# Kernel tuning notes

Hardware: AMD Instinct MI355X
Metric: run time of the kernel (lower is better)

## Reference

```python
import jax, jax.numpy as jnp
import numpy as np

N = 100000
E = 3200000
F_IN = 512
NUM_CLASSES = 8
H1, C1 = 4, 8   # conv1: 4 heads, 8 channels each (concat -> 32)
H2, C2 = 1, NUM_CLASSES  # conv2: 1 head, mean (concat=False)
NEG_SLOPE = 0.2


def gat_conv(x, W, att_src, att_dst, bias, src, dst, num_nodes, concat):
    """PyG-style GATConv (eval mode, self-loops already in src/dst)."""
    H, C = att_src.shape
    xp = (x @ W).reshape(-1, H, C)              # [N, H, C]
    a_s = (xp * att_src[None]).sum(-1)           # [N, H]
    a_d = (xp * att_dst[None]).sum(-1)           # [N, H]
    e = jax.nn.leaky_relu(a_s[src] + a_d[dst], NEG_SLOPE)  # [E, H]
    # segment softmax over destination nodes (stable)
    e_max = jax.ops.segment_max(e, dst, num_segments=num_nodes)
    e = jnp.exp(e - e_max[dst])
    denom = jax.ops.segment_sum(e, dst, num_segments=num_nodes)
    alpha = e / denom[dst]                        # [E, H]
    msg = xp[src] * alpha[..., None]              # [E, H, C]
    out = jax.ops.segment_sum(msg, dst, num_segments=num_nodes)  # [N, H, C]
    if concat:
        out = out.reshape(num_nodes, H * C)
    else:
        out = out.mean(axis=1)
    return out + bias


def setup_inputs() -> dict:
    key = jax.random.key(0)
    ks = jax.random.split(key, 9)
    s = 0.1
    return {
        "x": jax.random.normal(ks[0], (N, F_IN), dtype=jnp.float32),
        "edge_index": jax.random.randint(ks[1], (2, E), 0, N, dtype=jnp.int32),
        "W1": jax.random.normal(ks[2], (F_IN, H1 * C1), dtype=jnp.float32) * s,
        "att_src1": jax.random.normal(ks[3], (H1, C1), dtype=jnp.float32) * s,
        "att_dst1": jax.random.normal(ks[4], (H1, C1), dtype=jnp.float32) * s,
        "b1": jnp.zeros((H1 * C1,), dtype=jnp.float32),
        "W2": jax.random.normal(ks[5], (H1 * C1, H2 * C2), dtype=jnp.float32) * s,
        "att_src2": jax.random.normal(ks[6], (H2, C2), dtype=jnp.float32) * s,
        "att_dst2": jax.random.normal(ks[7], (H2, C2), dtype=jnp.float32) * s,
        "b2": jnp.zeros((C2,), dtype=jnp.float32),
    }


def reference(x, edge_index, W1, att_src1, att_dst1, b1, W2, att_src2, att_dst2, b2):
    # PyG GATConv default add_self_loops=True
    loop = jnp.arange(N, dtype=edge_index.dtype)
    src = jnp.concatenate([edge_index[0], loop])
    dst = jnp.concatenate([edge_index[1], loop])
    # dropout is identity in eval mode
    h = jax.nn.elu(gat_conv(x, W1, att_src1, att_dst1, b1, src, dst, N, True))
    out = gat_conv(h, W2, att_src2, att_dst2, b2, src, dst, N, False)
    return out
```

## Files before the change

### kernel.cpp

```cpp
#include <hip/hip_runtime.h>

typedef unsigned short u16;
typedef unsigned int   u32;

#define NN  100000
#define EE  3200000
#define ETOT 3300000
#define FIN 512
#define NBUK 1024
#define NPB  98
#define CAP  4096
#define TILE_A 2048
#define NBLK_A ((ETOT + TILE_A - 1) / TILE_A)
#define NBLK_G ((NN + 63) / 64)

typedef __attribute__((ext_vector_type(8))) short bfx8;
typedef __attribute__((ext_vector_type(4))) float f32x4;

__device__ __forceinline__ float bf2f(u16 u){ return __uint_as_float(((u32)u) << 16); }
__device__ __forceinline__ float lo16f(u32 v){ return __uint_as_float(v << 16); }
__device__ __forceinline__ float hi16f(u32 v){ return __uint_as_float(v & 0xffff0000u); }
__device__ __forceinline__ u16 f2bf(float f){
  u32 u = __float_as_uint(f);
  u += 0x7fffu + ((u >> 16) & 1u);
  return (u16)(u >> 16);
}
__device__ __forceinline__ u32 pack2(float a, float b){
  return ((u32)f2bf(b) << 16) | (u32)f2bf(a);
}

__device__ __forceinline__ void binA_body(int blk, const int* __restrict__ ei,
                                          u32* __restrict__ gcnt,
                                          u32* __restrict__ buk,
                                          u32* hcnt, u32* hbase){
  int t = threadIdx.x;
  hcnt[t] = 0; hcnt[t + 256] = 0; hcnt[t + 512] = 0; hcnt[t + 768] = 0;
  __syncthreads();
  int e0 = blk * TILE_A;
  u32 pk[8], meta[8];
  #pragma unroll
  for (int i = 0; i < 8; i++){
    int e = e0 + i*256 + t;
    if (e < ETOT){
      int s, d;
      if (e < EE){ s = ei[e]; d = ei[EE + e]; } else { s = e - EE; d = s; }
      u32 b = (u32)d / NPB;
      pk[i] = ((u32)(d - (int)b*NPB) << 17) | (u32)s;
      u32 r = atomicAdd(&hcnt[b], 1u);
      meta[i] = (b << 11) | r;
    } else meta[i] = 0xFFFFFFFFu;
  }
  __syncthreads();
  for (int q = t; q < NBUK; q += 256){
    u32 c = hcnt[q];
    if (c) hbase[q] = atomicAdd(&gcnt[q], c);
  }
  __syncthreads();
  #pragma unroll
  for (int i = 0; i < 8; i++){
    if (meta[i] != 0xFFFFFFFFu){
      u32 b = meta[i] >> 11, r = meta[i] & 2047u;
      buk[((u32)b << 12) + hbase[b] + r] = pk[i];
    }
  }
}

__device__ __forceinline__ void gemm_body(int gb,
    const float* __restrict__ x, const u16* __restrict__ WTb,
    const float* __restrict__ attS, const float* __restrict__ attD,
    u16* __restrict__ xp1, float* __restrict__ as1, float* __restrict__ ad1){
  int tid = threadIdx.x;
  int nb  = gb * 64;

  int lane = tid & 63, wid = tid >> 6;
  int m = lane & 15, quad = lane >> 4;
  int rowbase = wid * 16;
  int row = nb + rowbase + m; if (row >= NN) row = NN - 1;
  const float* xrow = x + (size_t)row * FIN + quad * 8;
  const u16* b0g = WTb + m * FIN + quad * 8;
  const u16* b1g = b0g + 16 * FIN;

  f32x4 acc0 = {0.f, 0.f, 0.f, 0.f};
  f32x4 acc1 = {0.f, 0.f, 0.f, 0.f};

  union Ubf { bfx8 v; u32 u[4]; };

  #pragma unroll
  for (int kc = 0; kc < 4; kc++){
    #pragma unroll
    for (int ks = 0; ks < 4; ks++){
      const float4* g = (const float4*)(xrow + kc*128 + ks*32);
      float4 f0 = g[0], f1 = g[1];
      Ubf ua;
      ua.u[0] = pack2(f0.x, f0.y); ua.u[1] = pack2(f0.z, f0.w);
      ua.u[2] = pack2(f1.x, f1.y); ua.u[3] = pack2(f1.z, f1.w);
      bfx8 b0 = *(const bfx8*)(b0g + kc*128 + ks*32);
      bfx8 b1 = *(const bfx8*)(b1g + kc*128 + ks*32);
      acc0 = __builtin_amdgcn_mfma_f32_16x16x32_bf16(ua.v, b0, acc0, 0, 0, 0);
      acc1 = __builtin_amdgcn_mfma_f32_16x16x32_bf16(ua.v, b1, acc1, 0, 0, 0);
    }
  }

  #pragma unroll
  for (int t = 0; t < 2; t++){
    f32x4 acc = t ? acc1 : acc0;
    int colg = t*16 + m;
    float aS = attS[colg], aD = attD[colg];
    #pragma unroll
    for (int r = 0; r < 4; r++){
      int node = nb + rowbase + quad*4 + r;
      float v = acc[r];
      if (node < NN) xp1[(size_t)node*32 + colg] = f2bf(v);
      float ps = v * aS, pd = v * aD;
      ps += __shfl_xor(ps, 1); ps += __shfl_xor(ps, 2); ps += __shfl_xor(ps, 4);
      pd += __shfl_xor(pd, 1); pd += __shfl_xor(pd, 2); pd += __shfl_xor(pd, 4);
      if ((m & 7) == 0 && node < NN){
        as1[node*4 + (colg >> 3)] = ps;
        ad1[node*4 + (colg >> 3)] = pd;
      }
    }
  }
}


__global__ void __launch_bounds__(256) k_fat(const int* __restrict__ ei,
    u32* __restrict__ gcnt, u32* __restrict__ buk,
    const float* __restrict__ x, const u16* __restrict__ WTb,
    const float* __restrict__ attS, const float* __restrict__ attD,
    u16* __restrict__ xp1, float* __restrict__ as1, float* __restrict__ ad1){
  __shared__ u32 sm[NBUK*2];
  if (blockIdx.x < NBLK_A)
    binA_body(blockIdx.x, ei, gcnt, buk, sm, sm + NBUK);
  else
    gemm_body(blockIdx.x - NBLK_A, x, WTb, attS, attD, xp1, as1, ad1);
}

__global__ void __launch_bounds__(256) k_binA(const int* __restrict__ ei,
                                              u32* __restrict__ gcnt,
                                              u32* __restrict__ buk){
  __shared__ u32 sm2[NBUK*2];
  binA_body(blockIdx.x, ei, gcnt, buk, sm2, sm2 + NBUK);
}

__global__ void __launch_bounds__(256) k_gemm1(
    const float* __restrict__ x, const u16* __restrict__ WTb,
    const float* __restrict__ attS, const float* __restrict__ attD,
    u16* __restrict__ xp1, float* __restrict__ as1, float* __restrict__ ad1){
  gemm_body(blockIdx.x, x, WTb, attS, attD, xp1, as1, ad1);
}

__global__ void __launch_bounds__(256) k_scatterB(const u32* __restrict__ gcnt,
                                                  const u32* __restrict__ buk,
                                                  int2* __restrict__ range,
                                                  int* __restrict__ srcs){
  __shared__ u32 dcnt[NPB + 1];
  __shared__ u32 cur[NPB];
  __shared__ u32 red[256];
  int b = blockIdx.x, t = threadIdx.x;
  u32 acc = 0;
  for (int i = t; i < b; i += 256) acc += gcnt[i];
  red[t] = acc;
  if (t < NPB + 1) dcnt[t] = 0;
  __syncthreads();
  for (int o = 128; o > 0; o >>= 1){
    if (t < o) red[t] += red[t + o];
    __syncthreads();
  }
  u32 gb = red[0];
  u32 lo = (u32)b << 12;
  u32 hi = lo + gcnt[b];
  for (u32 j = lo + t; j < hi; j += 256)
    atomicAdd(&dcnt[(buk[j] >> 17) + 1], 1u);
  __syncthreads();
  for (int o = 1; o < 128; o <<= 1){
    u32 x = 0;
    if (t < NPB + 1 && t >= o) x = dcnt[t - o];
    __syncthreads();
    if (t < NPB + 1 && t >= o) dcnt[t] += x;
    __syncthreads();
  }
  if (t < NPB){
    u32 beg = gb + dcnt[t];
    cur[t] = beg;
    int node = b * NPB + t;
    if (node < NN){
      range[node] = make_int2((int)beg, (int)(gb + dcnt[t + 1]));
    }
  }
  __syncthreads();
  for (u32 j = lo + t; j < hi; j += 256){
    u32 p = buk[j];
    u32 pos = atomicAdd(&cur[p >> 17], 1u);
    srcs[pos] = (int)(p & 0x1FFFFu);
  }
}

__global__ void k_prep_w(const float* __restrict__ W1, u16* __restrict__ WTb,
                         u32* __restrict__ gcnt){
  int i = blockIdx.x*blockDim.x + threadIdx.x;
  if (i < NBUK) gcnt[i] = 0;
  if (i >= FIN*32) return;
  int k = i >> 5, c = i & 31;
  WTb[c*FIN + k] = f2bf(W1[i]);
}

__global__ void __launch_bounds__(256) k_agg1(
    const int2* __restrict__ range, const int* __restrict__ srcs,
    const u32* __restrict__ xp1u, const float* __restrict__ as1,
    const float* __restrict__ ad1, const float* __restrict__ b1,
    u32* __restrict__ hfeatu){
  int wid = (blockIdx.x * 256 + threadIdx.x) >> 6;
  if (wid >= NN) return;
  int lane = threadIdx.x & 63;
  int e = lane >> 4;
  int l = lane & 15;
  int h = l >> 2;
  int2 rr = range[wid];
  int beg = rr.x, end = rr.y;
  float ad = ad1[wid*4 + h];
  float num0 = 0.f, num1 = 0.f, den = 0.f;
  int j = beg + e;
  for (; j + 12 < end; j += 16){
    int s0 = srcs[j], s1 = srcs[j + 4], s2 = srcs[j + 8], s3 = srcs[j + 12];
    u32 v0 = xp1u[(size_t)s0*16 + l];
    u32 v1 = xp1u[(size_t)s1*16 + l];
    u32 v2 = xp1u[(size_t)s2*16 + l];
    u32 v3 = xp1u[(size_t)s3*16 + l];
    float z0 = as1[s0*4 + h] + ad;
    float z1 = as1[s1*4 + h] + ad;
    float z2 = as1[s2*4 + h] + ad;
    float z3 = as1[s3*4 + h] + ad;
    z0 = (z0 >= 0.f) ? z0 : 0.2f * z0;
    z1 = (z1 >= 0.f) ? z1 : 0.2f * z1;
    z2 = (z2 >= 0.f) ? z2 : 0.2f * z2;
    z3 = (z3 >= 0.f) ? z3 : 0.2f * z3;
    float w0 = __expf(z0), w1 = __expf(z1), w2 = __expf(z2), w3 = __expf(z3);
    num0 = fmaf(w0, lo16f(v0), num0); num1 = fmaf(w0, hi16f(v0), num1); den += w0;
    num0 = fmaf(w1, lo16f(v1), num0); num1 = fmaf(w1, hi16f(v1), num1); den += w1;
    num0 = fmaf(w2, lo16f(v2), num0); num1 = fmaf(w2, hi16f(v2), num1); den += w2;
    num0 = fmaf(w3, lo16f(v3), num0); num1 = fmaf(w3, hi16f(v3), num1); den += w3;
  }
  if (j + 4 < end){
    int s0 = srcs[j], s1 = srcs[j + 4];
    u32 v0 = xp1u[(size_t)s0*16 + l];
    u32 v1 = xp1u[(size_t)s1*16 + l];
    float z0 = as1[s0*4 + h] + ad;
    float z1 = as1[s1*4 + h] + ad;
    z0 = (z0 >= 0.f) ? z0 : 0.2f * z0;
    z1 = (z1 >= 0.f) ? z1 : 0.2f * z1;
    float w0 = __expf(z0), w1 = __expf(z1);
    num0 = fmaf(w0, lo16f(v0), num0); num1 = fmaf(w0, hi16f(v0), num1); den += w0;
    num0 = fmaf(w1, lo16f(v1), num0); num1 = fmaf(w1, hi16f(v1), num1); den += w1;
    j += 8;
  }
  for (; j < end; j += 4){
    int s0 = srcs[j];
    u32 v0 = xp1u[(size_t)s0*16 + l];
    float z0 = as1[s0*4 + h] + ad;
    z0 = (z0 >= 0.f) ? z0 : 0.2f * z0;
    float w0 = __expf(z0);
    num0 = fmaf(w0, lo16f(v0), num0); num1 = fmaf(w0, hi16f(v0), num1); den += w0;
  }
  num0 += __shfl_xor(num0, 16); num0 += __shfl_xor(num0, 32);
  num1 += __shfl_xor(num1, 16); num1 += __shfl_xor(num1, 32);
  den  += __shfl_xor(den, 16);  den  += __shfl_xor(den, 32);
  if (e == 0){
    float o0 = num0 / den + b1[2*l];
    float o1 = num1 / den + b1[2*l + 1];
    o0 = (o0 > 0.f) ? o0 : (__expf(o0) - 1.f);
    o1 = (o1 > 0.f) ? o1 : (__expf(o1) - 1.f);
    hfeatu[(size_t)wid*16 + l] = pack2(o0, o1);
  }
}

__global__ void k_feat2(const u16* __restrict__ hfeat, const float* __restrict__ W2,
                        const float* __restrict__ attS, const float* __restrict__ attD,
                        float* __restrict__ xp2, float* __restrict__ as2,
                        float* __restrict__ ad2){
  int n = blockIdx.x*blockDim.x + threadIdx.x;
  if (n >= NN) return;
  const u16* hr = hfeat + (size_t)n*32;
  float h[32];
  #pragma unroll
  for (int k = 0; k < 32; k++) h[k] = bf2f(hr[k]);
  float o[8];
  #pragma unroll
  for (int j = 0; j < 8; j++) o[j] = 0.f;
  #pragma unroll
  for (int k = 0; k < 32; k++){
    #pragma unroll
    for (int j = 0; j < 8; j++) o[j] = fmaf(h[k], W2[k*8 + j], o[j]);
  }
  float s = 0.f, d = 0.f;
  #pragma unroll
  for (int j = 0; j < 8; j++){
    xp2[(size_t)n*8 + j] = o[j];
    s = fmaf(o[j], attS[j], s);
    d = fmaf(o[j], attD[j], d);
  }
  as2[n] = s; ad2[n] = d;
}

__global__ void __launch_bounds__(256) k_agg2(
    const int2* __restrict__ range, const int* __restrict__ srcs,
    const float* __restrict__ xp2, const float* __restrict__ as2,
    const float* __restrict__ ad2, const float* __restrict__ b2,
    float* __restrict__ out){
  int wid = (blockIdx.x * 256 + threadIdx.x) >> 6;
  if (wid >= NN) return;
  int lane = threadIdx.x & 63;
  int p = lane >> 3, c = lane & 7;
  int2 rr = range[wid];
  int beg = rr.x, end = rr.y;
  float ad = ad2[wid];
  float num = 0.f, den = 0.f;
  int j = beg + p;
  for (; j + 24 < end; j += 32){
    int s0 = srcs[j], s1 = srcs[j + 8], s2 = srcs[j + 16], s3 = srcs[j + 24];
    float v0 = xp2[(size_t)s0*8 + c];
    float v1 = xp2[(size_t)s1*8 + c];
    float v2 = xp2[(size_t)s2*8 + c];
    float v3 = xp2[(size_t)s3*8 + c];
    float z0 = as2[s0] + ad;
    float z1 = as2[s1] + ad;
    float z2 = as2[s2] + ad;
    float z3 = as2[s3] + ad;
    z0 = (z0 >= 0.f) ? z0 : 0.2f * z0;
    z1 = (z1 >= 0.f) ? z1 : 0.2f * z1;
    z2 = (z2 >= 0.f) ? z2 : 0.2f * z2;
    z3 = (z3 >= 0.f) ? z3 : 0.2f * z3;
    float w0 = __expf(z0), w1 = __expf(z1), w2 = __expf(z2), w3 = __expf(z3);
    num = fmaf(w0, v0, num); den += w0;
    num = fmaf(w1, v1, num); den += w1;
    num = fmaf(w2, v2, num); den += w2;
    num = fmaf(w3, v3, num); den += w3;
  }
  if (j + 8 < end){
    int s0 = srcs[j], s1 = srcs[j + 8];
    float v0 = xp2[(size_t)s0*8 + c];
    float v1 = xp2[(size_t)s1*8 + c];
    float z0 = as2[s0] + ad;
    float z1 = as2[s1] + ad;
    z0 = (z0 >= 0.f) ? z0 : 0.2f * z0;
    z1 = (z1 >= 0.f) ? z1 : 0.2f * z1;
    float w0 = __expf(z0), w1 = __expf(z1);
    num = fmaf(w0, v0, num); den += w0;
    num = fmaf(w1, v1, num); den += w1;
    j += 16;
  }
  for (; j < end; j += 8){
    int s0 = srcs[j];
    float v0 = xp2[(size_t)s0*8 + c];
    float z0 = as2[s0] + ad;
    z0 = (z0 >= 0.f) ? z0 : 0.2f * z0;
    float w0 = __expf(z0);
    num = fmaf(w0, v0, num); den += w0;
  }
  num += __shfl_xor(num, 8);  den += __shfl_xor(den, 8);
  num += __shfl_xor(num, 16); den += __shfl_xor(den, 16);
  num += __shfl_xor(num, 32); den += __shfl_xor(den, 32);
  if (p == 0){
    out[(size_t)wid*8 + c] = num / den + b2[c];
  }
}

extern "C" void kernel_launch(void* const* d_in, const int* in_sizes, int n_in,
                              void* d_out, int out_size, void* d_ws, size_t ws_size,
                              hipStream_t stream){
  (void)in_sizes; (void)n_in; (void)out_size;
  const float* x   = (const float*)d_in[0];
  const int*   ei  = (const int*)d_in[1];
  const float* W1  = (const float*)d_in[2];
  const float* aS1 = (const float*)d_in[3];
  const float* aD1 = (const float*)d_in[4];
  const float* b1  = (const float*)d_in[5];
  const float* W2  = (const float*)d_in[6];
  const float* aS2 = (const float*)d_in[7];
  const float* aD2 = (const float*)d_in[8];
  const float* b2  = (const float*)d_in[9];
  float* out = (float*)d_out;

  char* w = (char*)d_ws;
  auto alloc = [&](size_t bytes) -> char* {
    char* p = w; w += (bytes + 15) & ~(size_t)15; return p;
  };

  int2*  range  = (int2*)alloc((size_t)NN*8);
  int*   srcs   = (int*)alloc((size_t)ETOT*4);
  u16*   xp1    = (u16*)alloc((size_t)NN*64);
  float* as1    = (float*)alloc((size_t)NN*16);
  float* ad1    = (float*)alloc((size_t)NN*16);
  u16*   hfeat  = (u16*)alloc((size_t)NN*64);
  float* xp2    = (float*)alloc((size_t)NN*32);
  float* as2    = (float*)alloc((size_t)NN*4);
  float* ad2    = (float*)alloc((size_t)NN*4);
  u16*   WTb    = (u16*)alloc(32*512*2);
  u32*   gcnt   = (u32*)alloc(NBUK*4);
  size_t base_need = (size_t)(w - (char*)d_ws);
  size_t buk_bytes = (size_t)NBUK * CAP * 4;
  bool overlap = (ws_size >= base_need + buk_bytes);

  u32* buk;
  if (overlap){
    buk = (u32*)alloc(buk_bytes);
  } else {
    buk = (u32*)xp1;
  }

  k_prep_w  <<<64, 256, 0, stream>>>(W1, WTb, gcnt);
  if (overlap){
    k_fat   <<<NBLK_A + NBLK_G, 256, 0, stream>>>(ei, gcnt, buk, x, WTb, aS1, aD1,
                                                  xp1, as1, ad1);
    k_scatterB<<<NBUK, 256, 0, stream>>>(gcnt, buk, range, srcs);
  } else {
    k_binA  <<<NBLK_A, 256, 0, stream>>>(ei, gcnt, buk);
    k_scatterB<<<NBUK, 256, 0, stream>>>(gcnt, buk, range, srcs);
    k_gemm1 <<<NBLK_G, 256, 0, stream>>>(x, WTb, aS1, aD1, xp1, as1, ad1);
  }
  k_agg1    <<<NN/4, 256, 0, stream>>>(range, srcs, (const u32*)xp1, as1, ad1, b1, (u32*)hfeat);
  k_feat2   <<<(NN+255)/256, 256, 0, stream>>>(hfeat, W2, aS2, aD2, xp2, as2, ad2);
  k_agg2    <<<NN/4, 256, 0, stream>>>(range, srcs, xp2, as2, ad2, b2, out);
}
```

Measured before the change: 512.2 us.

## Enlarge binning tiles with two-pass count-then-scatter to cut global atomics

The edge-binning phase now processes eight times more edges per block. It first counts destination buckets in shared memory, then reserves global slots once per bucket, then re-reads the edges and scatters each one using a shared running offset. This reduces global atomicAdd traffic on the bucket counters and halves shared memory use. The cost is reading edge indices twice and having fewer, longer binning blocks to overlap with the GEMM blocks.

Result: no change. 510.4 us (-0.3%).

```diff
diff --git a/kernel.cpp b/kernel.cpp
--- a/kernel.cpp
+++ b/kernel.cpp
@@ -10,7 +10,7 @@
 #define NBUK 1024
 #define NPB  98
 #define CAP  4096
-#define TILE_A 2048
+#define TILE_A 16384
 #define NBLK_A ((ETOT + TILE_A - 1) / TILE_A)
 #define NBLK_G ((NN + 63) / 64)
 
@@ -32,35 +32,34 @@
 __device__ __forceinline__ void binA_body(int blk, const int* __restrict__ ei,
                                           u32* __restrict__ gcnt,
                                           u32* __restrict__ buk,
-                                          u32* hcnt, u32* hbase){
+                                          u32* hcnt){
   int t = threadIdx.x;
-  hcnt[t] = 0; hcnt[t + 256] = 0; hcnt[t + 512] = 0; hcnt[t + 768] = 0;
+  for (int q = t; q < NBUK; q += 256) hcnt[q] = 0;
   __syncthreads();
   int e0 = blk * TILE_A;
-  u32 pk[8], meta[8];
-  #pragma unroll
-  for (int i = 0; i < 8; i++){
+  #pragma unroll 4
+  for (int i = 0; i < TILE_A/256; i++){
+    int e = e0 + i*256 + t;
+    if (e < ETOT){
+      int d = (e < EE) ? ei[EE + e] : (e - EE);
+      atomicAdd(&hcnt[(u32)d / NPB], 1u);
+    }
+  }
+  __syncthreads();
+  for (int q = t; q < NBUK; q += 256){
+    u32 c = hcnt[q];
+    if (c) hcnt[q] = ((u32)q << 12) + atomicAdd(&gcnt[q], c);
+  }
+  __syncthreads();
+  #pragma unroll 4
+  for (int i = 0; i < TILE_A/256; i++){
     int e = e0 + i*256 + t;
     if (e < ETOT){
       int s, d;
       if (e < EE){ s = ei[e]; d = ei[EE + e]; } else { s = e - EE; d = s; }
       u32 b = (u32)d / NPB;
-      pk[i] = ((u32)(d - (int)b*NPB) << 17) | (u32)s;
       u32 r = atomicAdd(&hcnt[b], 1u);
-      meta[i] = (b << 11) | r;
-    } else meta[i] = 0xFFFFFFFFu;
-  }
-  __syncthreads();
-  for (int q = t; q < NBUK; q += 256){
-    u32 c = hcnt[q];
-    if (c) hbase[q] = atomicAdd(&gcnt[q], c);
-  }
-  __syncthreads();
-  #pragma unroll
-  for (int i = 0; i < 8; i++){
-    if (meta[i] != 0xFFFFFFFFu){
-      u32 b = meta[i] >> 11, r = meta[i] & 2047u;
-      buk[((u32)b << 12) + hbase[b] + r] = pk[i];
+      buk[r] = ((u32)(d - (int)b*NPB) << 17) | (u32)s;
     }
   }
 }
@@ -128,9 +127,9 @@
     const float* __restrict__ x, const u16* __restrict__ WTb,
     const float* __restrict__ attS, const float* __restrict__ attD,
     u16* __restrict__ xp1, float* __restrict__ as1, float* __restrict__ ad1){
-  __shared__ u32 sm[NBUK*2];
+  __shared__ u32 sm[NBUK];
   if (blockIdx.x < NBLK_A)
-    binA_body(blockIdx.x, ei, gcnt, buk, sm, sm + NBUK);
+    binA_body(blockIdx.x, ei, gcnt, buk, sm);
   else
     gemm_body(blockIdx.x - NBLK_A, x, WTb, attS, attD, xp1, as1, ad1);
 }
@@ -138,8 +137,8 @@
 __global__ void __launch_bounds__(256) k_binA(const int* __restrict__ ei,
                                               u32* __restrict__ gcnt,
                                               u32* __restrict__ buk){
-  __shared__ u32 sm2[NBUK*2];
-  binA_body(blockIdx.x, ei, gcnt, buk, sm2, sm2 + NBUK);
+  __shared__ u32 sm2[NBUK];
+  binA_body(blockIdx.x, ei, gcnt, buk, sm2);
 }
 
 __global__ void __launch_bounds__(256) k_gemm1(
```
